# Kernel optimization log

Hardware: AMD Instinct MI355X
Metric: run time of the kernel (lower is better)

The kernel has to match this reference:

```python
import jax, jax.numpy as jnp
import numpy as np

N_NODES = 50000
N_EDGES = 600000
N_GRAPHS = 64
IN_DIM = 6
HID = 128


def setup_inputs() -> dict:
    key = jax.random.key(0)
    ks = jax.random.split(key, 10)
    x = jax.random.normal(ks[0], (N_NODES, IN_DIM), dtype=jnp.float32)
    edge_index = jax.random.randint(ks[1], (2, N_EDGES), 0, N_NODES, dtype=jnp.int64)
    batch = jnp.sort(jax.random.randint(ks[2], (N_NODES,), 0, N_GRAPHS, dtype=jnp.int64))
    def glorot(k, shape):
        lim = float(np.sqrt(6.0 / (shape[0] + shape[1])))
        return jax.random.uniform(k, shape, jnp.float32, -lim, lim)
    return {
        'x': x, 'edge_index': edge_index, 'batch': batch,
        'W1': glorot(ks[3], (IN_DIM, HID)), 'b1': jnp.zeros((HID,), jnp.float32),
        'W2': glorot(ks[4], (HID, HID)), 'b2': jnp.zeros((HID,), jnp.float32),
        'W3': glorot(ks[5], (HID, HID)), 'b3': jnp.zeros((HID,), jnp.float32),
        'fc1_w': glorot(ks[6], (HID, 64)), 'fc1_b': jnp.zeros((64,), jnp.float32),
        'fc2_w': glorot(ks[7], (64, 1)), 'fc2_b': jnp.zeros((1,), jnp.float32),
    }


def _gcn_norm(edge_index, n):
    # PyG GCNConv default: add self-loops, symmetric D^-1/2 A D^-1/2 normalization.
    loop = jnp.arange(n, dtype=edge_index.dtype)
    src = jnp.concatenate([edge_index[0], loop])
    dst = jnp.concatenate([edge_index[1], loop])
    deg = jax.ops.segment_sum(jnp.ones_like(dst, dtype=jnp.float32), dst, num_segments=n)
    dis = jnp.where(deg > 0, jax.lax.rsqrt(jnp.maximum(deg, 1.0)), 0.0)
    norm = dis[src] * dis[dst]  # [E+N]
    return src, dst, norm


def _gcn_layer(x, W, b, src, dst, norm, n):
    h = x @ W                       # [N, H] small GEMM
    msg = h[src] * norm[:, None]    # [E+N, H] irregular gather
    out = jax.ops.segment_sum(msg, dst, num_segments=n)  # scatter-add
    return out + b


def reference(x, edge_index, batch, W1, b1, W2, b2, W3, b3, fc1_w, fc1_b, fc2_w, fc2_b):
    n = x.shape[0]
    src, dst, norm = _gcn_norm(edge_index, n)
    h = jax.nn.relu(_gcn_layer(x, W1, b1, src, dst, norm, n))
    h = jax.nn.relu(_gcn_layer(h, W2, b2, src, dst, norm, n))
    h = jax.nn.relu(_gcn_layer(h, W3, b3, src, dst, norm, n))
    # global mean pool over graphs
    sums = jax.ops.segment_sum(h, batch, num_segments=N_GRAPHS)  # [B, H]
    cnt = jax.ops.segment_sum(jnp.ones((n,), jnp.float32), batch, num_segments=N_GRAPHS)
    pooled = sums / jnp.maximum(cnt, 1.0)[:, None]
    z = jax.nn.relu(pooled @ fc1_w + fc1_b)
    return z @ fc2_w + fc2_b  # [B, 1]
```

## Files before the change

### kernel.cpp

```cpp
#include <hip/hip_runtime.h>
#include <hip/hip_fp16.h>

#define HID 128
#define NGRAPH 64
#define CAP 64

typedef unsigned int uint32;
typedef unsigned short ushort;
using short8 = __attribute__((ext_vector_type(8))) short;
using f32x4  = __attribute__((ext_vector_type(4))) float;

__device__ __forceinline__ float2 h2f2(uint32 u) {
    __half2 h = *(__half2*)&u;
    return __half22float2(h);
}
__device__ __forceinline__ uint32 f2h2(float a, float b) {
    __half2 h;
    h.x = __float2half(a);
    h.y = __float2half(b);
    return *(uint32*)&h;
}

__device__ __forceinline__ void accum4(float* acc, uint4 v) {
    float2 e0 = h2f2(v.x), e1 = h2f2(v.y), e2 = h2f2(v.z), e3 = h2f2(v.w);
    acc[0] += e0.x; acc[1] += e0.y; acc[2] += e1.x; acc[3] += e1.y;
    acc[4] += e2.x; acc[5] += e2.y; acc[6] += e3.x; acc[7] += e3.y;
}

__global__ void setup(int* __restrict__ fill, uint32* __restrict__ s1,
                      uint32* __restrict__ s2, float* __restrict__ pooled,
                      int n, int npool) {
    int i = blockIdx.x * blockDim.x + threadIdx.x;
    if (i < n) fill[i] = 0;
    if (i < 64) {
        s1[(size_t)n * 64 + i] = 0u;
        s2[(size_t)n * 64 + i] = 0u;
    }
    if (i < npool) pooled[i] = 0.f;
}

__global__ void csr_fill_pack(const int* __restrict__ src, const int* __restrict__ dst,
                              int* __restrict__ fill, int* __restrict__ csr,
                              int E, int EB,
                              const float* __restrict__ W2, const float* __restrict__ W3,
                              ushort* __restrict__ wt) {
    int b = blockIdx.x;
    if (b < EB) {
        int e = b * blockDim.x + threadIdx.x;
        if (e >= E) return;
        int d = dst[e];
        int pos = atomicAdd(&fill[d], 1);
        if (pos < CAP) csr[(size_t)d * CAP + pos] = src[e];
    } else {
        int t = (b - EB) * blockDim.x + threadIdx.x;
        int sel = t >> 14;
        int idx = t & 16383;
        int nn = idx >> 7, kk = idx & 127;
        const float* W = sel ? W3 : W2;
        wt[sel * 16384 + idx] = __half_as_ushort(__float2half(W[kk * HID + nn]));
    }
}

__global__ void finalize(const int* __restrict__ fill, float* __restrict__ dis,
                         const float* __restrict__ x, float4* __restrict__ xp4, int n) {
    int i = blockIdx.x * blockDim.x + threadIdx.x;
    if (i >= n) return;
    int d = fill[i] + 1;
    float di = (float)(1.0 / sqrt((double)d));
    dis[i] = di;
    const float* xi = x + (size_t)i * 6;
    xp4[(size_t)i * 2]     = make_float4(di * xi[0], di * xi[1], di * xi[2], di * xi[3]);
    xp4[(size_t)i * 2 + 1] = make_float4(di * xi[4], di * xi[5], 0.f, 0.f);
}

__global__ __launch_bounds__(256) void layer1_fused(
    const float4* __restrict__ xp4, const int* __restrict__ fill,
    const int* __restrict__ csr, const float* __restrict__ dis,
    const float* __restrict__ W1, const float* __restrict__ b1,
    uint32* __restrict__ S1, int n) {
    int t = blockIdx.x * blockDim.x + threadIdx.x;
    int i = t >> 6, lane = t & 63;
    if (i >= n) return;
    int m = fill[i]; if (m > CAP) m = CAP;
    float a0 = 0.f, a1 = 0.f, a2 = 0.f, a3 = 0.f, a4 = 0.f, a5 = 0.f;
    if (lane < m) {
        int s = csr[(size_t)i * CAP + lane];
        float4 p0 = xp4[(size_t)s * 2];
        float4 p1 = xp4[(size_t)s * 2 + 1];
        a0 = p0.x; a1 = p0.y; a2 = p0.z;
        a3 = p0.w; a4 = p1.x; a5 = p1.y;
    }
#pragma unroll
    for (int off = 32; off > 0; off >>= 1) {
        a0 += __shfl_xor(a0, off); a1 += __shfl_xor(a1, off);
        a2 += __shfl_xor(a2, off); a3 += __shfl_xor(a3, off);
        a4 += __shfl_xor(a4, off); a5 += __shfl_xor(a5, off);
    }
    float di = dis[i];
    float4 s0 = xp4[(size_t)i * 2];
    float4 s1 = xp4[(size_t)i * 2 + 1];
    float xa[6];
    xa[0] = di * (s0.x + a0); xa[1] = di * (s0.y + a1);
    xa[2] = di * (s0.z + a2); xa[3] = di * (s0.w + a3);
    xa[4] = di * (s1.x + a4); xa[5] = di * (s1.y + a5);
    int c0 = lane * 2;
    float z0 = b1[c0], z1 = b1[c0 + 1];
#pragma unroll
    for (int k = 0; k < 6; ++k) {
        z0 += xa[k] * W1[k * HID + c0];
        z1 += xa[k] * W1[k * HID + c0 + 1];
    }
    S1[(size_t)i * 64 + lane] = f2h2(di * fmaxf(z0, 0.f), di * fmaxf(z1, 0.f));
}

__global__ __launch_bounds__(256, 5) void layer_agg_gemm(
    const uint32* __restrict__ Sin, const int* __restrict__ fill,
    const int* __restrict__ csr, const float* __restrict__ dis,
    const ushort* __restrict__ WT, const float* __restrict__ bias,
    uint32* __restrict__ Sout, int n, int scaleOut) {
    __shared__ uint4 plds4[32 * 17];
    const int wave = threadIdx.x >> 6;
    const int lane = threadIdx.x & 63;
    const int grp = lane >> 4;
    const int q   = lane & 15;
    const int blk0 = blockIdx.x * 32;
    const int base = blk0 + wave * 8;

    int mt8[8];
    int idx8[8];
#pragma unroll
    for (int j = 0; j < 8; ++j) {
        int i = base + j;
        int fv = (i < n) ? fill[i] : 0;
        int m = fv > CAP ? CAP : fv;
        idx8[j] = (lane < m) ? csr[(size_t)i * CAP + lane]
                             : ((lane == m && i < n && m < CAP) ? i : n);
        mt8[j] = m + (m < CAP ? 1 : 0);
    }

#pragma unroll
    for (int jp = 0; jp < 4; ++jp) {
        const int ja = jp * 2, jb = ja + 1;
        float acca[8] = {0.f, 0.f, 0.f, 0.f, 0.f, 0.f, 0.f, 0.f};
        float accb[8] = {0.f, 0.f, 0.f, 0.f, 0.f, 0.f, 0.f, 0.f};
        {
            int sa1 = __shfl(idx8[ja], grp);
            int sa2 = __shfl(idx8[ja], 4 + grp);
            int sa3 = __shfl(idx8[ja], 8 + grp);
            int sa4 = __shfl(idx8[ja], 12 + grp);
            int sb1 = __shfl(idx8[jb], grp);
            int sb2 = __shfl(idx8[jb], 4 + grp);
            int sb3 = __shfl(idx8[jb], 8 + grp);
            int sb4 = __shfl(idx8[jb], 12 + grp);
            uint4 va1 = *(const uint4*)(Sin + (size_t)sa1 * 64 + q * 4);
            uint4 va2 = *(const uint4*)(Sin + (size_t)sa2 * 64 + q * 4);
            uint4 va3 = *(const uint4*)(Sin + (size_t)sa3 * 64 + q * 4);
            uint4 va4 = *(const uint4*)(Sin + (size_t)sa4 * 64 + q * 4);
            uint4 vb1 = *(const uint4*)(Sin + (size_t)sb1 * 64 + q * 4);
            uint4 vb2 = *(const uint4*)(Sin + (size_t)sb2 * 64 + q * 4);
            uint4 vb3 = *(const uint4*)(Sin + (size_t)sb3 * 64 + q * 4);
            uint4 vb4 = *(const uint4*)(Sin + (size_t)sb4 * 64 + q * 4);
            accum4(acca, va1); accum4(acca, va2);
            accum4(acca, va3); accum4(acca, va4);
            accum4(accb, vb1); accum4(accb, vb2);
            accum4(accb, vb3); accum4(accb, vb4);
        }
        for (int k = 16; k < mt8[ja]; k += 16) {
            int s1 = __shfl(idx8[ja], k + grp);
            int s2 = __shfl(idx8[ja], k + 4 + grp);
            int s3 = __shfl(idx8[ja], k + 8 + grp);
            int s4 = __shfl(idx8[ja], k + 12 + grp);
            uint4 v1 = *(const uint4*)(Sin + (size_t)s1 * 64 + q * 4);
            uint4 v2 = *(const uint4*)(Sin + (size_t)s2 * 64 + q * 4);
            uint4 v3 = *(const uint4*)(Sin + (size_t)s3 * 64 + q * 4);
            uint4 v4 = *(const uint4*)(Sin + (size_t)s4 * 64 + q * 4);
            accum4(acca, v1); accum4(acca, v2);
            accum4(acca, v3); accum4(acca, v4);
        }
        for (int k = 16; k < mt8[jb]; k += 16) {
            int s1 = __shfl(idx8[jb], k + grp);
            int s2 = __shfl(idx8[jb], k + 4 + grp);
            int s3 = __shfl(idx8[jb], k + 8 + grp);
            int s4 = __shfl(idx8[jb], k + 12 + grp);
            uint4 v1 = *(const uint4*)(Sin + (size_t)s1 * 64 + q * 4);
            uint4 v2 = *(const uint4*)(Sin + (size_t)s2 * 64 + q * 4);
            uint4 v3 = *(const uint4*)(Sin + (size_t)s3 * 64 + q * 4);
            uint4 v4 = *(const uint4*)(Sin + (size_t)s4 * 64 + q * 4);
            accum4(accb, v1); accum4(accb, v2);
            accum4(accb, v3); accum4(accb, v4);
        }
#pragma unroll
        for (int r = 0; r < 8; ++r) {
            acca[r] += __shfl_xor(acca[r], 16);
            acca[r] += __shfl_xor(acca[r], 32);
            accb[r] += __shfl_xor(accb[r], 16);
            accb[r] += __shfl_xor(accb[r], 32);
        }
        if (grp == 0) {
            int ia = base + ja, ib = base + jb;
            float da = (ia < n) ? dis[ia] : 0.f;
            float db = (ib < n) ? dis[ib] : 0.f;
            plds4[(wave * 8 + ja) * 17 + q] =
                make_uint4(f2h2(da * acca[0], da * acca[1]),
                           f2h2(da * acca[2], da * acca[3]),
                           f2h2(da * acca[4], da * acca[5]),
                           f2h2(da * acca[6], da * acca[7]));
            plds4[(wave * 8 + jb) * 17 + q] =
                make_uint4(f2h2(db * accb[0], db * accb[1]),
                           f2h2(db * accb[2], db * accb[3]),
                           f2h2(db * accb[4], db * accb[5]),
                           f2h2(db * accb[6], db * accb[7]));
        }
    }
    __syncthreads();

    const int l16 = lane & 15, quad = lane >> 4;
    f32x4 acc2[2][2] = {};
#pragma unroll
    for (int kc = 0; kc < 4; ++kc) {
        int ko = kc * 32 + quad * 8;
        short8 a0 = *(const short8*)&plds4[(size_t)l16 * 17 + kc * 4 + quad];
        short8 a1 = *(const short8*)&plds4[(size_t)(16 + l16) * 17 + kc * 4 + quad];
#pragma unroll
        for (int ct = 0; ct < 2; ++ct) {
            short8 wh = *(const short8*)(WT + (size_t)(wave * 32 + ct * 16 + l16) * HID + ko);
            acc2[0][ct] = __builtin_amdgcn_mfma_f32_16x16x32_f16(wh, a0, acc2[0][ct], 0, 0, 0);
            acc2[1][ct] = __builtin_amdgcn_mfma_f32_16x16x32_f16(wh, a1, acc2[1][ct], 0, 0, 0);
        }
    }
    ushort* so = (ushort*)Sout;
#pragma unroll
    for (int rt = 0; rt < 2; ++rt) {
        int node = blk0 + rt * 16 + l16;
        if (node >= n) continue;
        float sc = scaleOut ? dis[node] : 1.f;
#pragma unroll
        for (int ct = 0; ct < 2; ++ct) {
            int cb = wave * 32 + ct * 16 + quad * 4;
            float4 bv = *(const float4*)(bias + cb);
            float o0 = fmaxf(acc2[rt][ct][0] + bv.x, 0.f) * sc;
            float o1 = fmaxf(acc2[rt][ct][1] + bv.y, 0.f) * sc;
            float o2 = fmaxf(acc2[rt][ct][2] + bv.z, 0.f) * sc;
            float o3 = fmaxf(acc2[rt][ct][3] + bv.w, 0.f) * sc;
            *(uint2*)(so + (size_t)node * HID + cb) = make_uint2(f2h2(o0, o1), f2h2(o2, o3));
        }
    }
}

#define POOL_CHUNK 64
__global__ void pool_partial(const uint32* __restrict__ h, const int* __restrict__ batch,
                             float* __restrict__ pooled, int* __restrict__ gcnt, int n) {
    int c = threadIdx.x;
    int start = blockIdx.x * POOL_CHUNK;
    if (start >= n) return;
    int end = start + POOL_CHUNK;
    if (end > n) end = n;
    int curg = batch[start];
    float sx = 0.f, sy = 0.f;
    int cnt = 0;
    for (int i = start; i < end; ++i) {
        int g = batch[i];
        if (g != curg) {
            atomicAdd(&pooled[curg * HID + 2 * c], sx);
            atomicAdd(&pooled[curg * HID + 2 * c + 1], sy);
            if (c == 0) atomicAdd(&gcnt[curg], cnt);
            sx = 0.f; sy = 0.f; cnt = 0;
            curg = g;
        }
        float2 v = h2f2(h[(size_t)i * 64 + c]);
        sx += v.x; sy += v.y;
        ++cnt;
    }
    atomicAdd(&pooled[curg * HID + 2 * c], sx);
    atomicAdd(&pooled[curg * HID + 2 * c + 1], sy);
    if (c == 0) atomicAdd(&gcnt[curg], cnt);
}

__global__ void mlp_head(const float* __restrict__ pooled, const int* __restrict__ cnt,
                         const float* __restrict__ fc1w, const float* __restrict__ fc1b,
                         const float* __restrict__ fc2w, const float* __restrict__ fc2b,
                         float* __restrict__ out) {
    int g = blockIdx.x;
    int j = threadIdx.x;
    float inv = 1.0f / fmaxf((float)cnt[g], 1.0f);
    float z = fc1b[j];
    for (int k = 0; k < HID; ++k) z += (pooled[g * HID + k] * inv) * fc1w[k * 64 + j];
    z = fmaxf(z, 0.f);
    float v = z * fc2w[j];
#pragma unroll
    for (int off = 32; off > 0; off >>= 1) v += __shfl_down(v, off);
    if (j == 0) out[g] = v + fc2b[0];
}

extern "C" void kernel_launch(void* const* d_in, const int* in_sizes, int n_in,
                              void* d_out, int out_size, void* d_ws, size_t ws_size,
                              hipStream_t stream) {
    const float* x     = (const float*)d_in[0];
    const int*   ei    = (const int*)d_in[1];
    const int*   batch = (const int*)d_in[2];
    const float* W1    = (const float*)d_in[3];
    const float* b1    = (const float*)d_in[4];
    const float* W2    = (const float*)d_in[5];
    const float* b2    = (const float*)d_in[6];
    const float* W3    = (const float*)d_in[7];
    const float* b3    = (const float*)d_in[8];
    const float* fc1w  = (const float*)d_in[9];
    const float* fc1b  = (const float*)d_in[10];
    const float* fc2w  = (const float*)d_in[11];
    const float* fc2b  = (const float*)d_in[12];
    float* out = (float*)d_out;

    const int N = in_sizes[0] / 6;
    const int E = in_sizes[1] / 2;
    const int* src = ei;
    const int* dst = ei + E;

    char* ws = (char*)d_ws;
    char* p = ws;
    uint32* S1   = (uint32*)p;   p += (size_t)(N + 1) * 256;
    uint32* S2   = (uint32*)p;   p += (size_t)(N + 1) * 256;
    uint32* B1h  = (uint32*)p;   p += (size_t)N * 256;
    float4* xp4  = (float4*)p;   p += (size_t)N * 32;
    ushort* WT   = (ushort*)p;   p += 2 * 32768;
    float* dis     = (float*)p;  p += (size_t)N * 4;
    int*   fill    = (int*)p;    p += (size_t)N * 4;
    int*   csr     = (int*)p;    p += (size_t)N * CAP * 4;
    float* pooled  = (float*)p;  p += (size_t)NGRAPH * HID * 4;
    int*   gcnt    = (int*)p;

    const int B = 256;
    const int EB = (E + B - 1) / B;
    const int npool = NGRAPH * HID + NGRAPH;

    setup<<<(N + B - 1) / B, B, 0, stream>>>(fill, S1, S2, pooled, N, npool);
    csr_fill_pack<<<EB + 128, B, 0, stream>>>(src, dst, fill, csr, E, EB, W2, W3, WT);
    finalize<<<(N + B - 1) / B, B, 0, stream>>>(fill, dis, x, xp4, N);

    int nodeWaveBlocks = (int)(((size_t)N * 64 + B - 1) / B);
    int fusedBlocks = (N + 31) / 32;

    layer1_fused<<<nodeWaveBlocks, B, 0, stream>>>(xp4, fill, csr, dis, W1, b1, S1, N);

    layer_agg_gemm<<<fusedBlocks, B, 0, stream>>>(S1, fill, csr, dis, WT, b2, S2, N, 1);

    layer_agg_gemm<<<fusedBlocks, B, 0, stream>>>(S2, fill, csr, dis, WT + 16384, b3, B1h, N, 0);

    pool_partial<<<(N + POOL_CHUNK - 1) / POOL_CHUNK, 64, 0, stream>>>(B1h, batch, pooled, gcnt, N);

    mlp_head<<<NGRAPH, 64, 0, stream>>>(pooled, gcnt, fc1w, fc1b, fc2w, fc2b, out);
}
```

Before: 234.9 us.

## Fuse mean pooling and MLP head into one per-graph kernel without atomics

Replaces the chunked atomic pool kernel and the separate MLP head with a single kernel that uses one block per graph. Each block finds its node range by binary search on the sorted batch array, reduces its rows across four waves in shared memory, and then runs the MLP head. This removes the zeroing of the pooled buffer, the float atomics and one launch. The trade-off is only 64 blocks streaming the final activations, which may underuse the GPU's bandwidth.

Measured after the change: 236.5 us. About the same (+0.7%).

```diff
diff --git a/kernel.cpp b/kernel.cpp
--- a/kernel.cpp
+++ b/kernel.cpp
@@ -28,15 +28,13 @@
 }
 
 __global__ void setup(int* __restrict__ fill, uint32* __restrict__ s1,
-                      uint32* __restrict__ s2, float* __restrict__ pooled,
-                      int n, int npool) {
+                      uint32* __restrict__ s2, int n) {
     int i = blockIdx.x * blockDim.x + threadIdx.x;
     if (i < n) fill[i] = 0;
     if (i < 64) {
         s1[(size_t)n * 64 + i] = 0u;
         s2[(size_t)n * 64 + i] = 0u;
     }
-    if (i < npool) pooled[i] = 0.f;
 }
 
 __global__ void csr_fill_pack(const int* __restrict__ src, const int* __restrict__ dst,
@@ -247,49 +245,65 @@
     }
 }
 
-#define POOL_CHUNK 64
-__global__ void pool_partial(const uint32* __restrict__ h, const int* __restrict__ batch,
-                             float* __restrict__ pooled, int* __restrict__ gcnt, int n) {
-    int c = threadIdx.x;
-    int start = blockIdx.x * POOL_CHUNK;
-    if (start >= n) return;
-    int end = start + POOL_CHUNK;
-    if (end > n) end = n;
-    int curg = batch[start];
+__global__ __launch_bounds__(256) void pool_head(
+    const uint32* __restrict__ h, const int* __restrict__ batch,
+    const float* __restrict__ fc1w, const float* __restrict__ fc1b,
+    const float* __restrict__ fc2w, const float* __restrict__ fc2b,
+    float* __restrict__ out, int n) {
+    __shared__ float red[4][128];
+    __shared__ float pp[128];
+    const int g = blockIdx.x;
+    const int t = threadIdx.x;
+    const int sub = t >> 6, c = t & 63;
+
+    int lo0 = 0, hi0 = n, lo1 = 0, hi1 = n;
+    while (lo0 < hi0 || lo1 < hi1) {
+        if (lo0 < hi0) {
+            int mid = (lo0 + hi0) >> 1;
+            if (batch[mid] < g) lo0 = mid + 1; else hi0 = mid;
+        }
+        if (lo1 < hi1) {
+            int mid = (lo1 + hi1) >> 1;
+            if (batch[mid] < g + 1) lo1 = mid + 1; else hi1 = mid;
+        }
+    }
+    const int start = lo0, end = lo1;
+
     float sx = 0.f, sy = 0.f;
-    int cnt = 0;
-    for (int i = start; i < end; ++i) {
-        int g = batch[i];
-        if (g != curg) {
-            atomicAdd(&pooled[curg * HID + 2 * c], sx);
-            atomicAdd(&pooled[curg * HID + 2 * c + 1], sy);
-            if (c == 0) atomicAdd(&gcnt[curg], cnt);
-            sx = 0.f; sy = 0.f; cnt = 0;
-            curg = g;
-        }
+    int i = start + sub;
+    for (; i + 12 < end; i += 16) {
+        uint32 u0 = h[(size_t)i * 64 + c];
+        uint32 u1 = h[(size_t)(i + 4) * 64 + c];
+        uint32 u2 = h[(size_t)(i + 8) * 64 + c];
+        uint32 u3 = h[(size_t)(i + 12) * 64 + c];
+        float2 v0 = h2f2(u0), v1 = h2f2(u1), v2 = h2f2(u2), v3 = h2f2(u3);
+        sx += v0.x + v1.x + v2.x + v3.x;
+        sy += v0.y + v1.y + v2.y + v3.y;
+    }
+    for (; i < end; i += 4) {
         float2 v = h2f2(h[(size_t)i * 64 + c]);
         sx += v.x; sy += v.y;
-        ++cnt;
-    }
-    atomicAdd(&pooled[curg * HID + 2 * c], sx);
-    atomicAdd(&pooled[curg * HID + 2 * c + 1], sy);
-    if (c == 0) atomicAdd(&gcnt[curg], cnt);
-}
-
-__global__ void mlp_head(const float* __restrict__ pooled, const int* __restrict__ cnt,
-                         const float* __restrict__ fc1w, const float* __restrict__ fc1b,
-                         const float* __restrict__ fc2w, const float* __restrict__ fc2b,
-                         float* __restrict__ out) {
-    int g = blockIdx.x;
-    int j = threadIdx.x;
-    float inv = 1.0f / fmaxf((float)cnt[g], 1.0f);
-    float z = fc1b[j];
-    for (int k = 0; k < HID; ++k) z += (pooled[g * HID + k] * inv) * fc1w[k * 64 + j];
-    z = fmaxf(z, 0.f);
-    float v = z * fc2w[j];
-#pragma unroll
-    for (int off = 32; off > 0; off >>= 1) v += __shfl_down(v, off);
-    if (j == 0) out[g] = v + fc2b[0];
+    }
+    *(float2*)&red[sub][2 * c] = make_float2(sx, sy);
+    __syncthreads();
+
+    if (t < 64) {
+        float2 r0 = *(float2*)&red[0][2 * t];
+        float2 r1 = *(float2*)&red[1][2 * t];
+        float2 r2 = *(float2*)&red[2][2 * t];
+        float2 r3 = *(float2*)&red[3][2 * t];
+        float inv = 1.0f / fmaxf((float)(end - start), 1.0f);
+        pp[2 * t]     = (r0.x + r1.x + r2.x + r3.x) * inv;
+        pp[2 * t + 1] = (r0.y + r1.y + r2.y + r3.y) * inv;
+        float z = fc1b[t];
+#pragma unroll 8
+        for (int k = 0; k < HID; ++k) z += pp[k] * fc1w[k * 64 + t];
+        z = fmaxf(z, 0.f);
+        float v = z * fc2w[t];
+#pragma unroll
+        for (int off = 32; off > 0; off >>= 1) v += __shfl_down(v, off);
+        if (t == 0) out[g] = v + fc2b[0];
+    }
 }
 
 extern "C" void kernel_launch(void* const* d_in, const int* in_sizes, int n_in,
@@ -325,14 +339,11 @@
     float* dis     = (float*)p;  p += (size_t)N * 4;
     int*   fill    = (int*)p;    p += (size_t)N * 4;
     int*   csr     = (int*)p;    p += (size_t)N * CAP * 4;
-    float* pooled  = (float*)p;  p += (size_t)NGRAPH * HID * 4;
-    int*   gcnt    = (int*)p;
 
     const int B = 256;
     const int EB = (E + B - 1) / B;
-    const int npool = NGRAPH * HID + NGRAPH;
-
-    setup<<<(N + B - 1) / B, B, 0, stream>>>(fill, S1, S2, pooled, N, npool);
+
+    setup<<<(N + B - 1) / B, B, 0, stream>>>(fill, S1, S2, N);
     csr_fill_pack<<<EB + 128, B, 0, stream>>>(src, dst, fill, csr, E, EB, W2, W3, WT);
     finalize<<<(N + B - 1) / B, B, 0, stream>>>(fill, dis, x, xp4, N);
 
@@ -345,7 +356,5 @@
 
     layer_agg_gemm<<<fusedBlocks, B, 0, stream>>>(S2, fill, csr, dis, WT + 16384, b3, B1h, N, 0);
 
-    pool_partial<<<(N + POOL_CHUNK - 1) / POOL_CHUNK, 64, 0, stream>>>(B1h, batch, pooled, gcnt, N);
-
-    mlp_head<<<NGRAPH, 64, 0, stream>>>(pooled, gcnt, fc1w, fc1b, fc2w, fc2b, out);
-}
+    pool_head<<<NGRAPH, B, 0, stream>>>(B1h, batch, fc1w, fc1b, fc2w, fc2b, out, N);
+}
```
